# Kernel tuning notes

Hardware: AMD Instinct MI355X
Metric: run time of the kernel (lower is better)

## Reference

```python
import jax, jax.numpy as jnp
import numpy as np

HID = 50  # HIDDEN_SIZE in source


def _lstm_step(x, h, c, W_ih, W_hh, b):
    # PyTorch LSTM cell: gates order i, f, g, o
    gates = x @ W_ih.T + h @ W_hh.T + b  # [B, 4H]
    i, f, g, o = jnp.split(gates, 4, axis=-1)
    i = jax.nn.sigmoid(i)
    f = jax.nn.sigmoid(f)
    g = jnp.tanh(g)
    o = jax.nn.sigmoid(o)
    c = f * c + i * g
    h = o * jnp.tanh(c)
    return h, c


def setup_inputs() -> dict:
    key = jax.random.key(0)
    ks = jax.random.split(key, 11)
    B, S = 2048, 512
    H, I, O = HID, 1, 1
    s = 1.0 / np.sqrt(H)
    u = lambda k, shp: jax.random.uniform(k, shp, jnp.float32, -s, s)
    return {
        "source": jax.random.normal(ks[0], (B, S, I), jnp.float32),
        "enc_W_ih": u(ks[1], (4 * H, I)),
        "enc_W_hh": u(ks[2], (4 * H, H)),
        "enc_b_ih": u(ks[3], (4 * H,)),
        "enc_b_hh": u(ks[4], (4 * H,)),
        "dec_W_ih": u(ks[5], (4 * H, O)),
        "dec_W_hh": u(ks[6], (4 * H, H)),
        "dec_b_ih": u(ks[7], (4 * H,)),
        "dec_b_hh": u(ks[8], (4 * H,)),
        "fc_W": u(ks[9], (O, H)),
        "fc_b": u(ks[10], (O,)),
        "target_len": 256,
    }


def reference(source, enc_W_ih, enc_W_hh, enc_b_ih, enc_b_hh,
              dec_W_ih, dec_W_hh, dec_b_ih, dec_b_hh, fc_W, fc_b,
              target_len):
    B = source.shape[0]
    H = enc_W_hh.shape[1]
    dt = source.dtype
    h0 = jnp.zeros((B, H), dt)
    c0 = jnp.zeros((B, H), dt)

    enc_b = enc_b_ih + enc_b_hh

    def enc_step(carry, x_t):
        h, c = carry
        h, c = _lstm_step(x_t, h, c, enc_W_ih, enc_W_hh, enc_b)
        return (h, c), None

    # scan over time: [S, B, 1]
    (h, c), _ = jax.lax.scan(enc_step, (h0, c0), jnp.swapaxes(source, 0, 1))

    dec_b = dec_b_ih + dec_b_hh
    x0 = jnp.zeros((B, source.shape[2]), dt)  # decoder_input = zeros

    def dec_step(carry, _):
        x, h, c = carry
        h, c = _lstm_step(x, h, c, dec_W_ih, dec_W_hh, dec_b)
        y = h @ fc_W.T + fc_b  # [B, 1]
        return (y, h, c), y  # feed output back as next input

    _, ys = jax.lax.scan(dec_step, (x0, h, c), None, length=target_len)
    return jnp.swapaxes(ys, 0, 1)  # [B, target_len, 1]
```

## Files before the change

kernel.cpp:

```cpp
#include <hip/hip_runtime.h>


#define HID 50
#define SEQ 512
#define TGT 256
#define MB  4
#define NT  16
#define UPAD 72
#define L2E 1.44269504088896341f

typedef __attribute__((ext_vector_type(8))) _Float16 half8;
typedef __attribute__((ext_vector_type(4))) float f32x4;

__device__ __forceinline__ float sigm2(float a) {
    return __builtin_amdgcn_rcpf(1.0f + __builtin_amdgcn_exp2f(-a));
}
__device__ __forceinline__ float tanhc(float c) {
    return fmaf(2.0f,
        __builtin_amdgcn_rcpf(1.0f + __builtin_amdgcn_exp2f(-2.0f * L2E * c)),
        -1.0f);
}

#define MFMA16(A, B, C) __builtin_amdgcn_mfma_f32_16x16x32_f16((A), (B), (C), 0, 0, 0)

#define HS_S (MB * UPAD)
#define HS_SZ (2 * HS_S)

#define GSTEP(XV, IB, OB)                                                   \
    {                                                                       \
        const _Float16* hp_ = &hs[IB][as][ab][0];                           \
        half8 a0 = *(const half8*)(hp_ + kg * 8);             \
        half8 a1 = *(const half8*)(hp_ + 32 + kg * 8);        \
        float xv_ = (XV);                                                   \
        f32x4 acc[NT];                                                      \
        _Pragma("unroll")                                                   \
        for (int j = 0; j < NT; ++j) {                                      \
            f32x4 z = {0.0f, 0.0f, 0.0f, 0.0f};                             \
            z = MFMA16(a0, Bw[j][0], z);                                    \
            z = MFMA16(a1, Bw[j][1], z);                                    \
            acc[j] = z;                                                     \
        }                                                                   \
        _Float16* wp_ = &hs[OB][0][0][0];                                   \
        _Pragma("unroll")                                                   \
        for (int ug = 0; ug < 4; ++ug) {                                    \
            float sI = acc[0 * 4 + ug][0] + acc[0 * 4 + ug][2]              \
                     + fmaf(wx[0 * 4 + ug], xv_, bb[0 * 4 + ug]);           \
            float sF = acc[1 * 4 + ug][0] + acc[1 * 4 + ug][2]              \
                     + fmaf(wx[1 * 4 + ug], xv_, bb[1 * 4 + ug]);           \
            float sG = acc[2 * 4 + ug][0] + acc[2 * 4 + ug][2]              \
                     + fmaf(wx[2 * 4 + ug], xv_, bb[2 * 4 + ug]);           \
            float sO = acc[3 * 4 + ug][0] + acc[3 * 4 + ug][2]              \
                     + fmaf(wx[3 * 4 + ug], xv_, bb[3 * 4 + ug]);           \
            float vi = sigm2(sI);                                           \
            float vf = sigm2(sF);                                           \
            float vg = fmaf(2.0f, sigm2(sG), -1.0f);                        \
            float vo = sigm2(sO);                                           \
            cc[ug] = fmaf(vf, cc[ug], vi * vg);                             \
            hv[ug] = vo * tanhc(cc[ug]);                                    \
            _Float16 q0 = (_Float16)hv[ug];                                 \
            _Float16 q1 = (_Float16)(hv[ug] - (float)q0);                   \
            wp_[kg * UPAD + ug * 16 + c]        = q0;           \
            wp_[HS_S + kg * UPAD + ug * 16 + c] = q1;           \
        }                                                                   \
    }

#define DSTEP(T, IB, OB)                                                    \
    {                                                                       \
        GSTEP(xc, IB, OB)                                                   \
        float p = fmaf(fcw0, hv[0],                                         \
                  fmaf(fcw1, hv[1],                                         \
                  fmaf(fcw2, hv[2], fcw3 * hv[3])));                        \
        p += __shfl_xor(p, 1, 64);                                          \
        p += __shfl_xor(p, 2, 64);                                          \
        p += __shfl_xor(p, 4, 64);                                          \
        p += __shfl_xor(p, 8, 64);                                          \
        float y = p + fb;                                                   \
        if (c == 0) ys[kg][T] = y;                                          \
        xc = y;                                                             \
    }

extern "C" __global__ void __launch_bounds__(64, 1)
seq2seq_kernel(const float* __restrict__ src,
               const float* __restrict__ eWih, const float* __restrict__ eWhh,
               const float* __restrict__ eBih, const float* __restrict__ eBhh,
               const float* __restrict__ dWih, const float* __restrict__ dWhh,
               const float* __restrict__ dBih, const float* __restrict__ dBhh,
               const float* __restrict__ fcW, const float* __restrict__ fcB,
               float* __restrict__ out) {
    const int lane = threadIdx.x & 63;
    const int c    = lane & 15;
    const int kg   = lane >> 4;
    const int ab   = c >> 2;
    const int as   = (c >> 1) & 1;
    const int b0   = blockIdx.x * MB;

    __shared__ __align__(16) _Float16 hs[2][2][MB][UPAD];
    __shared__ __align__(16) float srcT[SEQ * MB];
    __shared__ __align__(16) float ys[MB][TGT];

    for (int i = lane; i < 2 * HS_SZ / 2; i += 64) ((int*)hs)[i] = 0;
    for (int i = lane; i < SEQ * MB; i += 64) {
        int e = i >> 9, t = i & 511;
        srcT[t * MB + e] = src[(size_t)(b0 + e) * SEQ + t];
    }

    half8 Bw[NT][2];
    float wx[NT], bb[NT];
    float cc[4] = {0.0f, 0.0f, 0.0f, 0.0f};
    float hv[4];

    auto loadW = [&](const float* Wih, const float* Whh,
                     const float* Bih, const float* Bhh) {
#pragma unroll
        for (int j = 0; j < NT; ++j) {
            const int g  = j >> 2, ug = j & 3;
            const int u  = ug * 16 + c;
            const bool uv = (u < HID);
            const float sc = (g == 2) ? 2.0f * L2E : L2E;
            const int row = g * HID + (uv ? u : 0);
            wx[j] = uv ? Wih[row] * sc : 0.0f;
            bb[j] = uv ? (Bih[row] + Bhh[row]) * sc : 0.0f;
#pragma unroll
            for (int kt = 0; kt < 2; ++kt) {
                half8 s0;
#pragma unroll
                for (int jj = 0; jj < 8; ++jj) {
                    int kk = kt * 32 + kg * 8 + jj;
                    float wv = (uv && kk < HID)
                             ? Whh[(size_t)row * HID + kk] * sc : 0.0f;
                    s0[jj] = (_Float16)wv;
                }
                Bw[j][kt] = s0;
            }
        }
    };

    loadW(eWih, eWhh, eBih, eBhh);
    for (int t = 0; t < SEQ; t += 2) {
        { GSTEP(srcT[t * MB + kg], 0, 1) }
        { GSTEP(srcT[(t + 1) * MB + kg], 1, 0) }
    }

    loadW(dWih, dWhh, dBih, dBhh);
    const float fcw0 = fcW[c];
    const float fcw1 = fcW[16 + c];
    const float fcw2 = fcW[32 + c];
    const float fcw3 = (48 + c < HID) ? fcW[48 + c] : 0.0f;
    const float fb   = fcB[0];
    float xc = 0.0f;
    for (int t = 0; t < TGT; t += 2) {
        DSTEP(t,     0, 1)
        DSTEP(t + 1, 1, 0)
    }

    for (int i = lane; i < MB * TGT; i += 64) {
        int b = i >> 8, t = i & 255;
        out[(size_t)(b0 + b) * TGT + t] = ys[b][t];
    }
}

extern "C" void kernel_launch(void* const* d_in, const int* in_sizes, int n_in,
                              void* d_out, int out_size, void* d_ws, size_t ws_size,
                              hipStream_t stream) {
    const float* src  = (const float*)d_in[0];
    const float* eWih = (const float*)d_in[1];
    const float* eWhh = (const float*)d_in[2];
    const float* eBih = (const float*)d_in[3];
    const float* eBhh = (const float*)d_in[4];
    const float* dWih = (const float*)d_in[5];
    const float* dWhh = (const float*)d_in[6];
    const float* dBih = (const float*)d_in[7];
    const float* dBhh = (const float*)d_in[8];
    const float* fcW  = (const float*)d_in[9];
    const float* fcB  = (const float*)d_in[10];
    float* out = (float*)d_out;

    const int B = in_sizes[0] / SEQ;
    seq2seq_kernel<<<B / MB, 64, 0, stream>>>(src, eWih, eWhh, eBih, eBhh,
                                              dWih, dWhh, dBih, dBhh,
                                              fcW, fcB, out);
}
```

Baseline: 591.7 us.

## Permute hidden-state LDS layout for vectorized stores and batch transcendentals

Reorders the hidden-unit index in shared memory (unit u stored at position (u%16)*4 + u/16) so each lane writes its four units as one half4 store instead of four scalar stores, and permutes the W_hh columns to match. The gate math is restructured so all exp2 and rcp calls for the 16 gates are issued in batches, giving the transcendental unit more independent work. The source is stored per batch row so two timesteps load as one float2. The trade-offs are a different LDS bank-access pattern for the A-fragment reads, and higher register pressure from keeping the 16 gate intermediates live at once.

```diff
diff --git a/kernel.cpp b/kernel.cpp
--- a/kernel.cpp
+++ b/kernel.cpp
@@ -6,32 +6,19 @@
 #define TGT 256
 #define MB  4
 #define NT  16
-#define UPAD 72
 #define L2E 1.44269504088896341f
 
 typedef __attribute__((ext_vector_type(8))) _Float16 half8;
+typedef __attribute__((ext_vector_type(4))) _Float16 half4;
 typedef __attribute__((ext_vector_type(4))) float f32x4;
 
-__device__ __forceinline__ float sigm2(float a) {
-    return __builtin_amdgcn_rcpf(1.0f + __builtin_amdgcn_exp2f(-a));
-}
-__device__ __forceinline__ float tanhc(float c) {
-    return fmaf(2.0f,
-        __builtin_amdgcn_rcpf(1.0f + __builtin_amdgcn_exp2f(-2.0f * L2E * c)),
-        -1.0f);
-}
-
 #define MFMA16(A, B, C) __builtin_amdgcn_mfma_f32_16x16x32_f16((A), (B), (C), 0, 0, 0)
-
-#define HS_S (MB * UPAD)
-#define HS_SZ (2 * HS_S)
 
 #define GSTEP(XV, IB, OB)                                                   \
     {                                                                       \
         const _Float16* hp_ = &hs[IB][as][ab][0];                           \
-        half8 a0 = *(const half8*)(hp_ + kg * 8);             \
-        half8 a1 = *(const half8*)(hp_ + 32 + kg * 8);        \
-        float xv_ = (XV);                                                   \
+        half8 a0 = *(const half8*)(hp_ + kg * 8);           \
+        half8 a1 = *(const half8*)(hp_ + 32 + kg * 8);      \
         f32x4 acc[NT];                                                      \
         _Pragma("unroll")                                                   \
         for (int j = 0; j < NT; ++j) {                                      \
@@ -40,28 +27,37 @@
             z = MFMA16(a1, Bw[j][1], z);                                    \
             acc[j] = z;                                                     \
         }                                                                   \
-        _Float16* wp_ = &hs[OB][0][0][0];                                   \
+        float xv_ = (XV);                                                   \
+        float s_[NT], E_[NT], R_[NT];                                       \
         _Pragma("unroll")                                                   \
-        for (int ug = 0; ug < 4; ++ug) {                                    \
-            float sI = acc[0 * 4 + ug][0] + acc[0 * 4 + ug][2]              \
-                     + fmaf(wx[0 * 4 + ug], xv_, bb[0 * 4 + ug]);           \
-            float sF = acc[1 * 4 + ug][0] + acc[1 * 4 + ug][2]              \
-                     + fmaf(wx[1 * 4 + ug], xv_, bb[1 * 4 + ug]);           \
-            float sG = acc[2 * 4 + ug][0] + acc[2 * 4 + ug][2]              \
-                     + fmaf(wx[2 * 4 + ug], xv_, bb[2 * 4 + ug]);           \
-            float sO = acc[3 * 4 + ug][0] + acc[3 * 4 + ug][2]              \
-                     + fmaf(wx[3 * 4 + ug], xv_, bb[3 * 4 + ug]);           \
-            float vi = sigm2(sI);                                           \
-            float vf = sigm2(sF);                                           \
-            float vg = fmaf(2.0f, sigm2(sG), -1.0f);                        \
-            float vo = sigm2(sO);                                           \
-            cc[ug] = fmaf(vf, cc[ug], vi * vg);                             \
-            hv[ug] = vo * tanhc(cc[ug]);                                    \
+        for (int j = 0; j < NT; ++j)                                        \
+            s_[j] = acc[j][0] + acc[j][2] + fmaf(wx[j], xv_, bb[j]);        \
+        _Pragma("unroll")                                                   \
+        for (int j = 0; j < NT; ++j)                                        \
+            E_[j] = __builtin_amdgcn_exp2f(-s_[j]);                         \
+        _Pragma("unroll")                                                   \
+        for (int j = 0; j < NT; ++j)                                        \
+            R_[j] = __builtin_amdgcn_rcpf(1.0f + E_[j]);                    \
+        float e2_[4], r2_[4];                                               \
+        _Pragma("unroll")                                                   \
+        for (int ug = 0; ug < 4; ++ug) {       \
+            float vg = fmaf(2.0f, R_[8 + ug], -1.0f);                       \
+            cc[ug] = fmaf(R_[4 + ug], cc[ug], R_[ug] * vg);                 \
+            e2_[ug] = __builtin_amdgcn_exp2f(-2.0f * L2E * cc[ug]);         \
+        }                                                                   \
+        _Pragma("unroll")                                                   \
+        for (int ug = 0; ug < 4; ++ug)                                      \
+            r2_[ug] = __builtin_amdgcn_rcpf(1.0f + e2_[ug]);                \
+        half4 w0_, w1_;                                                     \
+        _Pragma("unroll")                                                   \
+        for (int ug = 0; ug < 4; ++ug) {                  \
+            hv[ug] = R_[12 + ug] * fmaf(2.0f, r2_[ug], -1.0f);              \
             _Float16 q0 = (_Float16)hv[ug];                                 \
-            _Float16 q1 = (_Float16)(hv[ug] - (float)q0);                   \
-            wp_[kg * UPAD + ug * 16 + c]        = q0;           \
-            wp_[HS_S + kg * UPAD + ug * 16 + c] = q1;           \
+            w0_[ug] = q0;                                                   \
+            w1_[ug] = (_Float16)(hv[ug] - (float)q0);                       \
         }                                                                   \
+        *(half4*)&hs[OB][0][kg][c * 4] = w0_;              \
+        *(half4*)&hs[OB][1][kg][c * 4] = w1_;              \
     }
 
 #define DSTEP(T, IB, OB)                                                    \
@@ -94,14 +90,14 @@
     const int as   = (c >> 1) & 1;
     const int b0   = blockIdx.x * MB;
 
-    __shared__ __align__(16) _Float16 hs[2][2][MB][UPAD];
-    __shared__ __align__(16) float srcT[SEQ * MB];
+    __shared__ __align__(16) _Float16 hs[2][2][MB][64];
+    __shared__ __align__(16) float srcT[MB][SEQ];
     __shared__ __align__(16) float ys[MB][TGT];
 
-    for (int i = lane; i < 2 * HS_SZ / 2; i += 64) ((int*)hs)[i] = 0;
+    for (int i = lane; i < 2 * 2 * MB * 64 / 2; i += 64) ((int*)hs)[i] = 0;
     for (int i = lane; i < SEQ * MB; i += 64) {
         int e = i >> 9, t = i & 511;
-        srcT[t * MB + e] = src[(size_t)(b0 + e) * SEQ + t];
+        srcT[e][t] = src[(size_t)(b0 + e) * SEQ + t];
     }
 
     half8 Bw[NT][2];
@@ -126,8 +122,9 @@
 #pragma unroll
                 for (int jj = 0; jj < 8; ++jj) {
                     int kk = kt * 32 + kg * 8 + jj;
-                    float wv = (uv && kk < HID)
-                             ? Whh[(size_t)row * HID + kk] * sc : 0.0f;
+                    int us = (kk & 3) * 16 + (kk >> 2);
+                    float wv = (uv && us < HID)
+                             ? Whh[(size_t)row * HID + us] * sc : 0.0f;
                     s0[jj] = (_Float16)wv;
                 }
                 Bw[j][kt] = s0;
@@ -137,8 +134,9 @@
 
     loadW(eWih, eWhh, eBih, eBhh);
     for (int t = 0; t < SEQ; t += 2) {
-        { GSTEP(srcT[t * MB + kg], 0, 1) }
-        { GSTEP(srcT[(t + 1) * MB + kg], 1, 0) }
+        float2 xp = *(const float2*)&srcT[kg][t];
+        { GSTEP(xp.x, 0, 1) }
+        { GSTEP(xp.y, 1, 0) }
     }
 
     loadW(dWih, dWhh, dBih, dBhh);
```

Result: faster. 564.9 us (-4.5%).
